# Performance work log

Measured on AMD Instinct MI355X. Metric: run time of the kernel, lower is better.

The kernel has to match this reference:

```python
import jax, jax.numpy as jnp
import numpy as np

B, F_SP, F_DN, VOCAB, EMB = 16384, 26, 13, 100000, 16


def setup_inputs() -> dict:
    key = jax.random.key(0)
    ks = jax.random.split(key, 9)
    sparse_inputs = jax.random.randint(ks[0], (B, F_SP), 0, VOCAB, dtype=jnp.int32)
    dense_inputs = jax.random.normal(ks[1], (B, F_DN), dtype=jnp.float32)
    s = 0.02
    return {
        "sparse_inputs": sparse_inputs,
        "dense_inputs": dense_inputs,
        "linear_dense_W": jax.random.normal(ks[2], (F_DN, 1), jnp.float32) * s,
        "linear_dense_b": jnp.zeros((1,), jnp.float32),
        "linear_emb": jax.random.normal(ks[3], (F_SP, VOCAB, 1), jnp.float32) * s,  # per-feature 1-d linear embeddings
        "fm_emb": jax.random.normal(ks[4], (F_SP, VOCAB, EMB), jnp.float32) * s,    # per-feature FM embeddings
        "finish_W": jax.random.normal(ks[5], (1, 1), jnp.float32) * s,
        "finish_b": jnp.zeros((1,), jnp.float32),
        "like_W": jax.random.normal(ks[6], (1, 1), jnp.float32) * s,
        "like_b": jnp.zeros((1,), jnp.float32),
    }


def reference(sparse_inputs, dense_inputs, linear_dense_W, linear_dense_b,
              linear_emb, fm_emb, finish_W, finish_b, like_W, like_b):
    feat_idx = jnp.arange(F_SP)[None, :]  # [1, F]

    # first-order: dense linear + sum of 1-d sparse embeddings
    lin_dense = dense_inputs @ linear_dense_W + linear_dense_b          # [B, 1]
    lin_sparse = linear_emb[feat_idx, sparse_inputs]                    # [B, F, 1]
    first_order = lin_dense + jnp.sum(lin_sparse, axis=1)               # [B, 1]

    # second-order FM: 0.5 * sum((sum_f v)^2 - sum_f v^2)
    emb = fm_emb[feat_idx, sparse_inputs]                               # [B, F, E]
    summed = jnp.sum(emb, axis=1)                                       # [B, E]
    second_order = 0.5 * jnp.sum(summed * summed - jnp.sum(emb * emb, axis=1),
                                 axis=1, keepdims=True)                 # [B, 1]

    logits = first_order + second_order                                 # [B, 1]
    finish = jax.nn.sigmoid(logits @ finish_W + finish_b)               # [B, 1]
    like = jax.nn.sigmoid(logits @ like_W + like_b)                     # [B, 1]
    return jnp.concatenate([finish, like], axis=1)                      # [B, 2]
```

## Files before the change

### kernel.cpp

```cpp
#include <hip/hip_runtime.h>
#include <math.h>

#define B_TOT 16384
#define F_SP  26
#define F_DN  13
#define VOCAB 100000
#define EMB   16

__global__ __launch_bounds__(256) void fm_mtl_kernel(
    const int*   __restrict__ sparse,
    const float* __restrict__ dense,
    const float* __restrict__ ldW,
    const float* __restrict__ ldB,
    const float* __restrict__ lin_emb,
    const float* __restrict__ fm_emb,
    const float* __restrict__ fW,
    const float* __restrict__ fB,
    const float* __restrict__ lW,
    const float* __restrict__ lB,
    float*       __restrict__ out)
{
    __shared__ int s_idx[32 * F_SP];
    const int tid = threadIdx.x;
    const int block_base = blockIdx.x * 32;

    for (int i = tid; i < 32 * F_SP; i += 256)
        s_idx[i] = sparse[block_base * F_SP + i];
    __syncthreads();

    const int sloc = tid >> 3;
    const int g    = tid & 7;
    const int dc   = g & 3;
    const int fh   = g >> 2;
    const int b    = block_base + sloc;

    const int* idx = &s_idx[sloc * F_SP];

    float4 s = make_float4(0.f, 0.f, 0.f, 0.f);
    float ssq = 0.f;
    const int f0 = fh * 13;
    #pragma unroll
    for (int k = 0; k < 13; ++k) {
        const int f = f0 + k;
        const int v = idx[f];
        const float4 e = *reinterpret_cast<const float4*>(
            &fm_emb[((size_t)f * VOCAB + (size_t)v) * EMB + dc * 4]);
        s.x += e.x; s.y += e.y; s.z += e.z; s.w += e.w;
        ssq += e.x * e.x + e.y * e.y + e.z * e.z + e.w * e.w;
    }

    float lin = 0.f;
    if (dc == 0) {
        #pragma unroll
        for (int k = 0; k < 13; ++k) {
            const int f = f0 + k;
            const int v = idx[f];
            lin += lin_emb[(size_t)f * VOCAB + (size_t)v];
        }
        if (fh == 0) {
            float ld = ldB[0];
            #pragma unroll
            for (int j = 0; j < F_DN; ++j)
                ld += dense[b * F_DN + j] * ldW[j];
            lin += ld;
        }
    }

    s.x += __shfl_xor(s.x, 4);
    s.y += __shfl_xor(s.y, 4);
    s.z += __shfl_xor(s.z, 4);
    s.w += __shfl_xor(s.w, 4);

    const float p2 = s.x * s.x + s.y * s.y + s.z * s.z + s.w * s.w;
    float r = 0.25f * p2 - 0.5f * ssq + lin;
    r += __shfl_xor(r, 1);
    r += __shfl_xor(r, 2);
    r += __shfl_xor(r, 4);

    if (g == 0) {
        const float finish = 1.f / (1.f + expf(-(r * fW[0] + fB[0])));
        const float like   = 1.f / (1.f + expf(-(r * lW[0] + lB[0])));
        *reinterpret_cast<float2*>(&out[b * 2]) = make_float2(finish, like);
    }
}

extern "C" void kernel_launch(void* const* d_in, const int* in_sizes, int n_in,
                              void* d_out, int out_size, void* d_ws, size_t ws_size,
                              hipStream_t stream) {
    const int*   sparse  = (const int*)  d_in[0];
    const float* dense   = (const float*)d_in[1];
    const float* ldW     = (const float*)d_in[2];
    const float* ldB     = (const float*)d_in[3];
    const float* lin_emb = (const float*)d_in[4];
    const float* fm_emb  = (const float*)d_in[5];
    const float* fW      = (const float*)d_in[6];
    const float* fB      = (const float*)d_in[7];
    const float* lW      = (const float*)d_in[8];
    const float* lB      = (const float*)d_in[9];
    float* out = (float*)d_out;

    dim3 grid(B_TOT / 32);
    dim3 block(256);
    fm_mtl_kernel<<<grid, block, 0, stream>>>(
        sparse, dense, ldW, ldB, lin_emb, fm_emb, fW, fB, lW, lB, out);
}
```

Before: 21.89 us.

## Use 16 lanes per sample with float2 gathers and spread linear terms

Each sample now gets 16 threads instead of 8. Each thread gathers float2 slices of the FM embedding rather than float4, and the grid doubles to 1024 blocks of 16 samples each. The serial linear-embedding and dense-dot loops, which only one or two lanes ran before, are spread across all 16 lanes with one or two loads per lane. The aim is more memory-level parallelism and less lane imbalance, in exchange for narrower loads and one extra shuffle stage.

```diff
diff --git a/kernel.cpp b/kernel.cpp
--- a/kernel.cpp
+++ b/kernel.cpp
@@ -20,62 +20,52 @@
     const float* __restrict__ lB,
     float*       __restrict__ out)
 {
-    __shared__ int s_idx[32 * F_SP];
+    __shared__ int s_idx[16 * F_SP];
     const int tid = threadIdx.x;
-    const int block_base = blockIdx.x * 32;
+    const int block_base = blockIdx.x * 16;
 
-    for (int i = tid; i < 32 * F_SP; i += 256)
+    for (int i = tid; i < 16 * F_SP; i += 256)
         s_idx[i] = sparse[block_base * F_SP + i];
     __syncthreads();
 
-    const int sloc = tid >> 3;
-    const int g    = tid & 7;
-    const int dc   = g & 3;
-    const int fh   = g >> 2;
+    const int sloc = tid >> 4;
+    const int g    = tid & 15;
+    const int d    = g & 7;
+    const int fh   = g >> 3;
     const int b    = block_base + sloc;
 
     const int* idx = &s_idx[sloc * F_SP];
 
-    float4 s = make_float4(0.f, 0.f, 0.f, 0.f);
+    float lin = lin_emb[(size_t)g * VOCAB + (size_t)idx[g]];
+    if (g < 10)
+        lin += lin_emb[(size_t)(g + 16) * VOCAB + (size_t)idx[g + 16]];
+    if (g < F_DN)
+        lin += dense[b * F_DN + g] * ldW[g];
+    if (g == 0)
+        lin += ldB[0];
+
+    float2 s = make_float2(0.f, 0.f);
     float ssq = 0.f;
     const int f0 = fh * 13;
     #pragma unroll
     for (int k = 0; k < 13; ++k) {
         const int f = f0 + k;
         const int v = idx[f];
-        const float4 e = *reinterpret_cast<const float4*>(
-            &fm_emb[((size_t)f * VOCAB + (size_t)v) * EMB + dc * 4]);
-        s.x += e.x; s.y += e.y; s.z += e.z; s.w += e.w;
-        ssq += e.x * e.x + e.y * e.y + e.z * e.z + e.w * e.w;
+        const float2 e = *reinterpret_cast<const float2*>(
+            &fm_emb[((size_t)f * VOCAB + (size_t)v) * EMB + d * 2]);
+        s.x += e.x; s.y += e.y;
+        ssq += e.x * e.x + e.y * e.y;
     }
 
-    float lin = 0.f;
-    if (dc == 0) {
-        #pragma unroll
-        for (int k = 0; k < 13; ++k) {
-            const int f = f0 + k;
-            const int v = idx[f];
-            lin += lin_emb[(size_t)f * VOCAB + (size_t)v];
-        }
-        if (fh == 0) {
-            float ld = ldB[0];
-            #pragma unroll
-            for (int j = 0; j < F_DN; ++j)
-                ld += dense[b * F_DN + j] * ldW[j];
-            lin += ld;
-        }
-    }
+    s.x += __shfl_xor(s.x, 8);
+    s.y += __shfl_xor(s.y, 8);
 
-    s.x += __shfl_xor(s.x, 4);
-    s.y += __shfl_xor(s.y, 4);
-    s.z += __shfl_xor(s.z, 4);
-    s.w += __shfl_xor(s.w, 4);
-
-    const float p2 = s.x * s.x + s.y * s.y + s.z * s.z + s.w * s.w;
+    const float p2 = s.x * s.x + s.y * s.y;
     float r = 0.25f * p2 - 0.5f * ssq + lin;
     r += __shfl_xor(r, 1);
     r += __shfl_xor(r, 2);
     r += __shfl_xor(r, 4);
+    r += __shfl_xor(r, 8);
 
     if (g == 0) {
         const float finish = 1.f / (1.f + expf(-(r * fW[0] + fB[0])));
@@ -99,7 +89,7 @@
     const float* lB      = (const float*)d_in[9];
     float* out = (float*)d_out;
 
-    dim3 grid(B_TOT / 32);
+    dim3 grid(B_TOT / 16);
     dim3 block(256);
     fm_mtl_kernel<<<grid, block, 0, stream>>>(
         sparse, dense, ldW, ldB, lin_emb, fm_emb, fW, fB, lW, lB, out);
```

After: 20.64 us. 1.06x faster.
